# Performance work log

Measured on AMD Instinct MI355X. Metric: run time of the kernel, lower is better.

Reference implementation:

```python
import jax, jax.numpy as jnp
import numpy as np

N = 20000      # nodes
E = 160000     # edges
IN = 128       # in_channels
H = 16         # heads
C = 32         # hidden_channels (per-head dim)
HC = H * C     # 512
ED = 93        # edge_dim
B = 64         # graphs in batch


def setup_inputs() -> dict:
    key = jax.random.key(0)
    ks = jax.random.split(key, 32)
    w = lambda i, shape: jax.random.normal(ks[i], shape, dtype=jnp.float32) * 0.05
    inp = {
        "x": jax.random.normal(ks[0], (N, IN), dtype=jnp.float32),
        "edge_attr": jax.random.normal(ks[1], (E, ED), dtype=jnp.float32),
        "edge_index": jax.random.randint(ks[2], (2, E), 0, N),
        # sorted batch assignment; every graph id 0..B-1 is present
        "batch": (jnp.arange(N) * B) // N,
        # transformer1: in=IN
        "t1_Wq": w(3, (IN, HC)), "t1_bq": jnp.zeros((HC,), jnp.float32),
        "t1_Wk": w(4, (IN, HC)), "t1_bk": jnp.zeros((HC,), jnp.float32),
        "t1_Wv": w(5, (IN, HC)), "t1_bv": jnp.zeros((HC,), jnp.float32),
        "t1_We": w(6, (ED, HC)),
        "t1_Ws": w(7, (IN, HC)), "t1_bs": jnp.zeros((HC,), jnp.float32),
        # transformer2: in=HC
        "t2_Wq": w(8, (HC, HC)), "t2_bq": jnp.zeros((HC,), jnp.float32),
        "t2_Wk": w(9, (HC, HC)), "t2_bk": jnp.zeros((HC,), jnp.float32),
        "t2_Wv": w(10, (HC, HC)), "t2_bv": jnp.zeros((HC,), jnp.float32),
        "t2_We": w(11, (ED, HC)),
        "t2_Ws": w(12, (HC, HC)), "t2_bs": jnp.zeros((HC,), jnp.float32),
        # MLP head: fc1 (hidden*32 -> hidden*8), fc2 (hidden*8 -> hidden)
        "fc1_W": w(13, (2 * HC, 8 * C)), "fc1_b": jnp.zeros((8 * C,), jnp.float32),
        "fc2_W": w(14, (8 * C, C)), "fc2_b": jnp.zeros((C,), jnp.float32),
    }
    return inp


def _tconv(x, src, dst, edge_attr, Wq, bq, Wk, bk, Wv, bv, We, Ws, bs):
    # PyG TransformerConv, concat=True, beta=False, root_weight=True
    n = x.shape[0]
    q = (x @ Wq + bq).reshape(n, H, C)
    k = (x @ Wk + bk).reshape(n, H, C)
    v = (x @ Wv + bv).reshape(n, H, C)
    e = (edge_attr @ We).reshape(-1, H, C)          # lin_edge has no bias
    kj = k[src] + e                                  # [E,H,C]
    alpha = jnp.einsum('ehc,ehc->eh', q[dst], kj) / jnp.sqrt(jnp.float32(C))
    # segment softmax over incoming edges of each destination node
    amax = jax.ops.segment_max(alpha, dst, num_segments=n)
    ex = jnp.exp(alpha - amax[dst])
    denom = jax.ops.segment_sum(ex, dst, num_segments=n)
    a = ex / denom[dst]                              # [E,H]
    msg = (v[src] + e) * a[:, :, None]               # [E,H,C]
    agg = jax.ops.segment_sum(msg.reshape(-1, HC), dst, num_segments=n)
    return agg + x @ Ws + bs                         # root/skip connection


def _pool(x, batch):
    counts = jax.ops.segment_sum(jnp.ones((x.shape[0],), x.dtype), batch, num_segments=B)
    mean = jax.ops.segment_sum(x, batch, num_segments=B) / jnp.maximum(counts, 1.0)[:, None]
    mx = jax.ops.segment_max(x, batch, num_segments=B)
    return jnp.concatenate([mean, mx], axis=1)


def reference(x, edge_attr, edge_index, batch,
              t1_Wq, t1_bq, t1_Wk, t1_bk, t1_Wv, t1_bv, t1_We, t1_Ws, t1_bs,
              t2_Wq, t2_bq, t2_Wk, t2_bk, t2_Wv, t2_bv, t2_We, t2_Ws, t2_bs,
              fc1_W, fc1_b, fc2_W, fc2_b):
    src, dst = edge_index[0], edge_index[1]
    x1 = jax.nn.leaky_relu(_tconv(x, src, dst, edge_attr,
                                  t1_Wq, t1_bq, t1_Wk, t1_bk, t1_Wv, t1_bv,
                                  t1_We, t1_Ws, t1_bs), negative_slope=0.2)
    x3 = _pool(x1, batch)
    x2 = jax.nn.leaky_relu(_tconv(x1, src, dst, edge_attr,
                                  t2_Wq, t2_bq, t2_Wk, t2_bk, t2_Wv, t2_bv,
                                  t2_We, t2_Ws, t2_bs), negative_slope=0.2)
    x4 = _pool(x2, batch)
    h = x3 + x4                                      # [B, 2*HC]
    h = jax.nn.relu(h @ fc1_W + fc1_b)               # dropout = identity (eval)
    out = h @ fc2_W + fc2_b                          # [B, C]
    return out
```

## Files before the change

### kernel.cpp

```cpp
#include <hip/hip_runtime.h>
#include <cstdint>
#include <cstddef>

#define N_NODES 20000
#define N_EDGES 160000
#define IN_CH   128
#define NH      16
#define CD      32
#define HC      512
#define ED      93
#define EDP     96
#define NB      64
#define NCAT    2048
#define NSLICE  8

typedef __attribute__((ext_vector_type(8))) short short8;
typedef __attribute__((ext_vector_type(4))) float f32x4;
typedef unsigned short ushort_t;


__device__ inline ushort_t f2bf(float f) {
    unsigned int u = __float_as_uint(f);
    u = (u + 0x7FFF + ((u >> 16) & 1)) >> 16;
    return (ushort_t)u;
}
__device__ inline float bf2f(ushort_t u) {
    return __uint_as_float((unsigned)u << 16);
}
__device__ inline void unpack8(uint4 u, float* o) {
    o[0] = bf2f((ushort_t)(u.x & 0xffff)); o[1] = bf2f((ushort_t)(u.x >> 16));
    o[2] = bf2f((ushort_t)(u.y & 0xffff)); o[3] = bf2f((ushort_t)(u.y >> 16));
    o[4] = bf2f((ushort_t)(u.z & 0xffff)); o[5] = bf2f((ushort_t)(u.z >> 16));
    o[6] = bf2f((ushort_t)(u.w & 0xffff)); o[7] = bf2f((ushort_t)(u.w >> 16));
}
__device__ inline uint4 packf8(const float* f) {
    uint4 u;
    u.x = (unsigned)f2bf(f[0]) | ((unsigned)f2bf(f[1]) << 16);
    u.y = (unsigned)f2bf(f[2]) | ((unsigned)f2bf(f[3]) << 16);
    u.z = (unsigned)f2bf(f[4]) | ((unsigned)f2bf(f[5]) << 16);
    u.w = (unsigned)f2bf(f[6]) | ((unsigned)f2bf(f[7]) << 16);
    return u;
}

__device__ inline void gload_lds16(const void* g, void* l) {
    __builtin_amdgcn_global_load_lds(
        (const __attribute__((address_space(1))) void*)g,
        (__attribute__((address_space(3))) void*)l, 16, 0, 0);
}

__global__ void k_fill(float* __restrict__ p, float v, int n) {
    int i = blockIdx.x * blockDim.x + threadIdx.x;
    int stride = gridDim.x * blockDim.x;
    for (; i < n; i += stride) p[i] = v;
}
__global__ void k_zero_i(int* __restrict__ p, int n) {
    int i = blockIdx.x * blockDim.x + threadIdx.x;
    int stride = gridDim.x * blockDim.x;
    for (; i < n; i += stride) p[i] = 0;
}

__global__ void k_cvt_x(const float* __restrict__ in, ushort_t* __restrict__ out, int n8) {
    int i = blockIdx.x * blockDim.x + threadIdx.x;
    int stride = gridDim.x * blockDim.x;
    for (; i < n8; i += stride) {
        const float4* p = (const float4*)(in + (size_t)i * 8);
        float4 a = p[0], b = p[1];
        float f[8] = {a.x, a.y, a.z, a.w, b.x, b.y, b.z, b.w};
        *(uint4*)(out + (size_t)i * 8) = packf8(f);
    }
}

__global__ void k_cvt_ea(const float* __restrict__ in, ushort_t* __restrict__ out) {
    int i = blockIdx.x * blockDim.x + threadIdx.x;
    int stride = gridDim.x * blockDim.x;
    int total = N_EDGES * EDP;
    for (; i < total; i += stride) {
        int m = i / EDP, k = i - m * EDP;
        out[i] = (k < ED) ? f2bf(in[(size_t)m * ED + k]) : (ushort_t)0;
    }
}

__global__ __launch_bounds__(256) void k_cvt_wtT(
    const float* __restrict__ W0, const float* __restrict__ W1,
    const float* __restrict__ W2, const float* __restrict__ W3,
    ushort_t* __restrict__ Wt, int K, int N, int Kp) {
    __shared__ float tile[32][33];
    int z = blockIdx.z;
    const float* W = (z == 0) ? W0 : (z == 1) ? W1 : (z == 2) ? W2 : W3;
    ushort_t* out = Wt + (size_t)z * N * Kp;
    int n0 = blockIdx.x << 5;
    int k0 = blockIdx.y << 5;
    int r = threadIdx.x >> 5;
    int c = threadIdx.x & 31;
#pragma unroll
    for (int rr = 0; rr < 4; ++rr) {
        int k = k0 + r + rr * 8;
        tile[r + rr * 8][c] = (k < K) ? W[(size_t)k * N + n0 + c] : 0.f;
    }
    __syncthreads();
#pragma unroll
    for (int rr = 0; rr < 4; ++rr) {
        int n = n0 + r + rr * 8;
        out[(size_t)n * Kp + k0 + c] = f2bf(tile[c][r + rr * 8]);
    }
}

__global__ void k_bcat2(
    const float* __restrict__ b0q, const float* __restrict__ b0k,
    const float* __restrict__ b0v, const float* __restrict__ b0s,
    const float* __restrict__ b1q, const float* __restrict__ b1k,
    const float* __restrict__ b1v, const float* __restrict__ b1s,
    float* __restrict__ out) {
    int i = blockIdx.x * blockDim.x + threadIdx.x;
    if (i >= 2 * NCAT) return;
    int l = i >> 11, j = i & (NCAT - 1);
    int s = j >> 9, jj = j & 511;
    const float* b = (l == 0)
        ? ((s == 0) ? b0q : (s == 1) ? b0k : (s == 2) ? b0v : b0s)
        : ((s == 0) ? b1q : (s == 1) ? b1k : (s == 2) ? b1v : b1s);
    out[i] = b[jj];
}


__global__ void k_hist(const int* __restrict__ dst, int* __restrict__ deg) {
    int i = blockIdx.x * blockDim.x + threadIdx.x;
    if (i < N_EDGES) atomicAdd(&deg[dst[i]], 1);
}

__global__ __launch_bounds__(1024) void k_scan(const int* __restrict__ deg,
                                               int* __restrict__ rowptr,
                                               int* __restrict__ cursor) {
    __shared__ int part[1024];
    int t = threadIdx.x;
    int base = t * 20;
    int loc[20];
    int s = 0;
#pragma unroll
    for (int i = 0; i < 20; ++i) {
        int idx = base + i;
        int v = (idx < N_NODES) ? deg[idx] : 0;
        loc[i] = s; s += v;
    }
    part[t] = s;
    __syncthreads();
    for (int off = 1; off < 1024; off <<= 1) {
        int v = (t >= off) ? part[t - off] : 0;
        __syncthreads();
        part[t] += v;
        __syncthreads();
    }
    int pre = (t > 0) ? part[t - 1] : 0;
#pragma unroll
    for (int i = 0; i < 20; ++i) {
        int idx = base + i;
        if (idx < N_NODES) {
            int v = pre + loc[i];
            rowptr[idx] = v;
            cursor[idx] = v;
        }
    }
    if (t == 1023) rowptr[N_NODES] = part[1023];
}

__global__ void k_scatter(const int* __restrict__ src, const int* __restrict__ dst,
                          int* __restrict__ cursor, int* __restrict__ perm,
                          int* __restrict__ psrc) {
    int i = blockIdx.x * blockDim.x + threadIdx.x;
    if (i >= N_EDGES) return;
    int d = dst[i];
    int p = atomicAdd(&cursor[d], 1);
    perm[p] = i;
    psrc[p] = src[i];
}


__global__ __launch_bounds__(256) void k_mfma_gemm(
    const ushort_t* __restrict__ A, const ushort_t* __restrict__ Bt,
    const float* __restrict__ bias, ushort_t* __restrict__ Yb,
    int M, int K, int N) {
    __shared__ char smem[32768];
    char* As = smem;
    char* Bs = smem + 16384;

    int tid  = threadIdx.x;
    int lane = tid & 63, wave = tid >> 6;
    int l15 = lane & 15, lg = lane >> 4;
    int nt = N >> 7;
    int nwg = gridDim.x;
    int bid = blockIdx.x;
    int wg;
    if ((nwg & 7) == 0) { int cpx = nwg >> 3; wg = (bid & 7) * cpx + (bid >> 3); }
    else wg = bid;
    int bm = (wg / nt) * 128, bn = (wg % nt) * 128;
    int wm = (wave >> 1) * 64, wn = (wave & 1) * 64;

    f32x4 acc[4][4] = {};

    int sr = lane >> 3;
    int su = lane & 7;
    int gu = su ^ sr;

    for (int k0 = 0; k0 < K; k0 += 64) {
#pragma unroll
        for (int i = 0; i < 4; ++i) {
            int rloc = wave * 32 + i * 8;
            int row = rloc + sr;
            if (bm + row < M)
                gload_lds16(A + (size_t)(bm + row) * K + k0 + gu * 8, As + rloc * 128);
            gload_lds16(Bt + (size_t)(bn + row) * K + k0 + gu * 8, Bs + rloc * 128);
        }
        __syncthreads();

#pragma unroll
        for (int ks = 0; ks < 2; ++ks) {
            short8 af[4], bfr[4];
#pragma unroll
            for (int mr = 0; mr < 4; ++mr) {
                int r = wm + mr * 16 + l15;
                af[mr] = *(const short8*)(As + r * 128 + (((ks * 4 + lg) ^ (r & 7)) << 4));
            }
#pragma unroll
            for (int nc = 0; nc < 4; ++nc) {
                int r = wn + nc * 16 + l15;
                bfr[nc] = *(const short8*)(Bs + r * 128 + (((ks * 4 + lg) ^ (r & 7)) << 4));
            }
#pragma unroll
            for (int mr = 0; mr < 4; ++mr)
#pragma unroll
                for (int nc = 0; nc < 4; ++nc)
                    acc[mr][nc] = __builtin_amdgcn_mfma_f32_16x16x32_bf16(
                        af[mr], bfr[nc], acc[mr][nc], 0, 0, 0);
        }
        __syncthreads();
    }

    char* Cs = smem;
#pragma unroll
    for (int mr = 0; mr < 4; ++mr) {
#pragma unroll
        for (int nc = 0; nc < 4; ++nc) {
            int coll = wn + nc * 16 + l15;
            float b = bias ? bias[bn + coll] : 0.f;
            int u0 = coll >> 3;
#pragma unroll
            for (int j = 0; j < 4; ++j) {
                int row = wm + mr * 16 + lg * 4 + j;
                int u = u0 ^ (row & 7);
                *(ushort_t*)(Cs + row * 256 + (u << 4) + ((coll & 7) << 1)) =
                    f2bf(acc[mr][nc][j] + b);
            }
        }
    }
    __syncthreads();
    {
        int rsub = tid >> 4;
        int un   = tid & 15;
#pragma unroll
        for (int i = 0; i < 8; ++i) {
            int row = i * 16 + rsub;
            int gr = bm + row;
            if (gr < M) {
                int u = un ^ (row & 7);
                *(uint4*)(Yb + (size_t)gr * N + bn + un * 8) =
                    *(const uint4*)(Cs + row * 256 + (u << 4));
            }
        }
    }
}


__global__ __launch_bounds__(256) void k_egemm(
    const ushort_t* __restrict__ Ab, const ushort_t* __restrict__ Bt,
    ushort_t* __restrict__ Yb, const int* __restrict__ perm,
    int pbase, int ec) {
    __shared__ char smem[49152];
    char* As = smem;
    char* Bs = smem + 24576;

    int tid  = threadIdx.x;
    int lane = tid & 63, wave = tid >> 6;
    int l15 = lane & 15, lg = lane >> 4;
    int nwg = gridDim.x;
    int bid = blockIdx.x;
    int wg;
    if ((nwg & 7) == 0) { int cpx = nwg >> 3; wg = (bid & 7) * cpx + (bid >> 3); }
    else wg = bid;
    int bm = (wg >> 2) * 128;
    int n0 = (wg & 3) * 128;
    int wm = (wave >> 1) * 64, wn = (wave & 1) * 64;

    int srow = tid >> 1;
    int h    = tid & 1;
    int ssw  = ((srow >> 1) & 3) << 4;
    {
        int gm = bm + srow;
        uint4 va[6];
#pragma unroll
        for (int i = 0; i < 6; ++i) { va[i].x = va[i].y = va[i].z = va[i].w = 0; }
        if (gm < ec) {
            int ar = perm[pbase + gm];
            const uint4* ga = (const uint4*)(Ab + (size_t)ar * EDP + h * 48);
#pragma unroll
            for (int i = 0; i < 6; ++i) va[i] = ga[i];
        }
        char* dsta = As + srow * 192;
#pragma unroll
        for (int i = 0; i < 6; ++i) {
            int c = h * 96 + i * 16;
            *(uint4*)(dsta + ((c & ~63) | ((c & 63) ^ ssw))) = va[i];
        }
        uint4 vb[6];
        {
            const uint4* gb = (const uint4*)(Bt + (size_t)(n0 + srow) * EDP + h * 48);
#pragma unroll
            for (int i = 0; i < 6; ++i) vb[i] = gb[i];
        }
        char* dstb = Bs + srow * 192;
#pragma unroll
        for (int i = 0; i < 6; ++i) {
            int c = h * 96 + i * 16;
            *(uint4*)(dstb + ((c & ~63) | ((c & 63) ^ ssw))) = vb[i];
        }
    }
    __syncthreads();

    int fsw = ((l15 >> 1) & 3) << 4;

    f32x4 acc[4][4] = {};
#pragma unroll
    for (int ks = 0; ks < 3; ++ks) {
        short8 af[4], bfr[4];
#pragma unroll
        for (int mr = 0; mr < 4; ++mr) {
            int r = wm + mr * 16 + l15;
            int c = ks * 64 + ((lg * 16) ^ fsw);
            af[mr] = *(const short8*)(As + r * 192 + c);
        }
#pragma unroll
        for (int nc = 0; nc < 4; ++nc) {
            int r = wn + nc * 16 + l15;
            int c = ks * 64 + ((lg * 16) ^ fsw);
            bfr[nc] = *(const short8*)(Bs + r * 192 + c);
        }
#pragma unroll
        for (int mr = 0; mr < 4; ++mr)
#pragma unroll
            for (int nc = 0; nc < 4; ++nc)
                acc[mr][nc] = __builtin_amdgcn_mfma_f32_16x16x32_bf16(
                    af[mr], bfr[nc], acc[mr][nc], 0, 0, 0);
    }
    __syncthreads();

    char* Cs = smem;
#pragma unroll
    for (int mr = 0; mr < 4; ++mr) {
#pragma unroll
        for (int nc = 0; nc < 4; ++nc) {
            int col = wn + nc * 16 + l15;
#pragma unroll
            for (int j = 0; j < 4; ++j) {
                int row = wm + mr * 16 + lg * 4 + j;
                *(ushort_t*)(Cs + row * 288 + col * 2) = f2bf(acc[mr][nc][j]);
            }
        }
    }
    __syncthreads();

    {
        int rsub = tid >> 4;
        int un   = tid & 15;
#pragma unroll
        for (int i = 0; i < 8; ++i) {
            int row = i * 16 + rsub;
            if (bm + row < ec) {
                *(uint4*)(Yb + (size_t)(bm + row) * HC + n0 + un * 8) =
                    *(const uint4*)(Cs + row * 288 + un * 16);
            }
        }
    }
}


__global__ __launch_bounds__(128) void k_edge_f(
    const ushort_t* __restrict__ qkvs, const ushort_t* __restrict__ eb,
    const int* __restrict__ psrc, const int* __restrict__ rowptr,
    ushort_t* __restrict__ xoutb) {
    int n = blockIdx.x;
    int beg = rowptr[n], end = rowptr[n + 1];

    int t = threadIdx.x;
    int w = t >> 6;
    int lane = t & 63;
    int c0 = lane * 8;
    int h = lane >> 2;

    float q[8];
    unpack8(*(const uint4*)(qkvs + (size_t)n * NCAT + c0), q);

    float mm = -1e30f, dd = 0.f, a[8];
#pragma unroll
    for (int j = 0; j < 8; ++j) a[j] = 0.f;

    int i = beg + w;
    uint4 ku4, vu4, eu4;
    if (i < end) {
        int sn = psrc[i];
        ku4 = *(const uint4*)(qkvs + (size_t)sn * NCAT + 512 + c0);
        vu4 = *(const uint4*)(qkvs + (size_t)sn * NCAT + 1024 + c0);
        eu4 = *(const uint4*)(eb + (size_t)i * HC + c0);
    }
    while (i < end) {
        uint4 kc = ku4, vc = vu4, ec = eu4;
        int inext = i + 2;
        if (inext < end) {
            int sn2 = psrc[inext];
            ku4 = *(const uint4*)(qkvs + (size_t)sn2 * NCAT + 512 + c0);
            vu4 = *(const uint4*)(qkvs + (size_t)sn2 * NCAT + 1024 + c0);
            eu4 = *(const uint4*)(eb + (size_t)inext * HC + c0);
        }
        float kk[8], vv[8], ee[8];
        unpack8(kc, kk); unpack8(vc, vv); unpack8(ec, ee);
        float part = 0.f;
#pragma unroll
        for (int j = 0; j < 8; ++j) part += q[j] * (kk[j] + ee[j]);
        part += __shfl_xor(part, 1);
        part += __shfl_xor(part, 2);
        float s = part * 0.17677669529663687f;
        float mn = fmaxf(mm, s);
        float sc = __expf(mm - mn);
        float p  = __expf(s - mn);
        dd = dd * sc + p;
        mm = mn;
#pragma unroll
        for (int j = 0; j < 8; ++j) a[j] = a[j] * sc + p * (vv[j] + ee[j]);
        i = inext;
    }

    __shared__ float sm_acc[512];
    __shared__ float sm_m[16];
    __shared__ float sm_d[16];
    if (w == 1) {
#pragma unroll
        for (int j = 0; j < 8; ++j) sm_acc[c0 + j] = a[j];
        if ((lane & 3) == 0) { sm_m[h] = mm; sm_d[h] = dd; }
    }
    __syncthreads();
    if (w == 0) {
        float m1 = sm_m[h], d1 = sm_d[h];
        float M = fmaxf(mm, m1);
        float sc0 = __expf(mm - M);
        float sc1 = __expf(m1 - M);
        dd = dd * sc0 + d1 * sc1;
        float inv = (dd > 0.f) ? 1.f / dd : 0.f;
        float sk[8];
        unpack8(*(const uint4*)(qkvs + (size_t)n * NCAT + 1536 + c0), sk);
        float o[8];
#pragma unroll
        for (int j = 0; j < 8; ++j) {
            float msg = (a[j] * sc0 + sm_acc[c0 + j] * sc1) * inv;
            float v = msg + sk[j];
            o[j] = v >= 0.f ? v : 0.2f * v;
        }
        *(uint4*)(xoutb + (size_t)n * HC + c0) = packf8(o);
    }
}

__global__ __launch_bounds__(128) void k_edge(
    const ushort_t* __restrict__ qkvs, const ushort_t* __restrict__ eb,
    const int* __restrict__ psrc, const int* __restrict__ rowptr,
    float* __restrict__ macc, float* __restrict__ mbuf, float* __restrict__ dbuf,
    int e0, int e1) {
    int n = blockIdx.x;
    int beg = rowptr[n], end = rowptr[n + 1];
    int lo = beg > e0 ? beg : e0;
    int hi = end < e1 ? end : e1;
    if (lo >= hi) return;

    int t = threadIdx.x;
    int w = t >> 6;
    int lane = t & 63;
    int c0 = lane * 8;
    int h = lane >> 2;
    bool fresh = (beg >= e0);

    float q[8];
    unpack8(*(const uint4*)(qkvs + (size_t)n * NCAT + c0), q);

    float mm, dd, a[8];
    if (w == 0 && !fresh) {
        mm = mbuf[n * NH + h];
        dd = dbuf[n * NH + h];
        float4 a0 = *(const float4*)(macc + (size_t)n * HC + c0);
        float4 a1 = *(const float4*)(macc + (size_t)n * HC + c0 + 4);
        a[0] = a0.x; a[1] = a0.y; a[2] = a0.z; a[3] = a0.w;
        a[4] = a1.x; a[5] = a1.y; a[6] = a1.z; a[7] = a1.w;
    } else {
        mm = -1e30f; dd = 0.f;
#pragma unroll
        for (int j = 0; j < 8; ++j) a[j] = 0.f;
    }

    int i = lo + w;
    uint4 ku4, vu4, eu4;
    if (i < hi) {
        int sn = psrc[i];
        ku4 = *(const uint4*)(qkvs + (size_t)sn * NCAT + 512 + c0);
        vu4 = *(const uint4*)(qkvs + (size_t)sn * NCAT + 1024 + c0);
        eu4 = *(const uint4*)(eb + (size_t)(i - e0) * HC + c0);
    }
    while (i < hi) {
        uint4 kc = ku4, vc = vu4, ec = eu4;
        int inext = i + 2;
        if (inext < hi) {
            int sn2 = psrc[inext];
            ku4 = *(const uint4*)(qkvs + (size_t)sn2 * NCAT + 512 + c0);
            vu4 = *(const uint4*)(qkvs + (size_t)sn2 * NCAT + 1024 + c0);
            eu4 = *(const uint4*)(eb + (size_t)(inext - e0) * HC + c0);
        }
        float kk[8], vv[8], ee[8];
        unpack8(kc, kk); unpack8(vc, vv); unpack8(ec, ee);
        float part = 0.f;
#pragma unroll
        for (int j = 0; j < 8; ++j) part += q[j] * (kk[j] + ee[j]);
        part += __shfl_xor(part, 1);
        part += __shfl_xor(part, 2);
        float s = part * 0.17677669529663687f;
        float mn = fmaxf(mm, s);
        float sc = __expf(mm - mn);
        float p  = __expf(s - mn);
        dd = dd * sc + p;
        mm = mn;
#pragma unroll
        for (int j = 0; j < 8; ++j) a[j] = a[j] * sc + p * (vv[j] + ee[j]);
        i = inext;
    }

    __shared__ float sm_acc[512];
    __shared__ float sm_m[16];
    __shared__ float sm_d[16];
    if (w == 1) {
#pragma unroll
        for (int j = 0; j < 8; ++j) sm_acc[c0 + j] = a[j];
        if ((lane & 3) == 0) { sm_m[h] = mm; sm_d[h] = dd; }
    }
    __syncthreads();
    if (w == 0) {
        float m1 = sm_m[h], d1 = sm_d[h];
        float M = fmaxf(mm, m1);
        float sc0 = __expf(mm - M);
        float sc1 = __expf(m1 - M);
        dd = dd * sc0 + d1 * sc1;
        float4 o0, o1;
        o0.x = a[0] * sc0 + sm_acc[c0 + 0] * sc1;
        o0.y = a[1] * sc0 + sm_acc[c0 + 1] * sc1;
        o0.z = a[2] * sc0 + sm_acc[c0 + 2] * sc1;
        o0.w = a[3] * sc0 + sm_acc[c0 + 3] * sc1;
        o1.x = a[4] * sc0 + sm_acc[c0 + 4] * sc1;
        o1.y = a[5] * sc0 + sm_acc[c0 + 5] * sc1;
        o1.z = a[6] * sc0 + sm_acc[c0 + 6] * sc1;
        o1.w = a[7] * sc0 + sm_acc[c0 + 7] * sc1;
        *(float4*)(macc + (size_t)n * HC + c0) = o0;
        *(float4*)(macc + (size_t)n * HC + c0 + 4) = o1;
        if ((lane & 3) == 0) { mbuf[n * NH + h] = M; dbuf[n * NH + h] = dd; }
    }
}

__global__ void k_epi2(const float* __restrict__ macc, const float* __restrict__ dbuf,
                       const ushort_t* __restrict__ qkvs, ushort_t* __restrict__ xoutb,
                       int n) {
    int i = blockIdx.x * blockDim.x + threadIdx.x;
    int stride = gridDim.x * blockDim.x;
    for (; i < n; i += stride) {
        int node = i >> 9, c = i & (HC - 1);
        int h = c >> 5;
        float dd = dbuf[node * NH + h];
        float msg = (dd > 0.f) ? macc[i] / dd : 0.f;
        float sk = bf2f(qkvs[(size_t)node * NCAT + 1536 + c]);
        float v = msg + sk;
        v = v >= 0.f ? v : 0.2f * v;
        xoutb[i] = f2bf(v);
    }
}


__global__ __launch_bounds__(256) void k_pool2(
    const ushort_t* __restrict__ xb, const int* __restrict__ batch,
    float* __restrict__ psum_p, float* __restrict__ pmax_p, int* __restrict__ cnt) {
    int b = blockIdx.x;
    int s = blockIdx.y;
    int lo = 0, hi = N_NODES;
    while (lo < hi) { int mid = (lo + hi) >> 1; if (batch[mid] < b) lo = mid + 1; else hi = mid; }
    int beg = lo;
    hi = N_NODES;
    while (lo < hi) { int mid = (lo + hi) >> 1; if (batch[mid] < b + 1) lo = mid + 1; else hi = mid; }
    int end = lo;
    if (s == 0 && threadIdx.x == 0) cnt[b] = end - beg;
    int cn = end - beg;
    int per = (cn + NSLICE - 1) / NSLICE;
    int nb = beg + s * per;
    int ne = nb + per; if (ne > end) ne = end;
    int c0 = threadIdx.x * 2;
    float s0 = 0.f, s1 = 0.f, m0 = -1e30f, m1 = -1e30f;
    for (int n = nb; n < ne; ++n) {
        unsigned int v = *(const unsigned int*)(xb + (size_t)n * HC + c0);
        float v0 = bf2f((ushort_t)(v & 0xffff));
        float v1 = bf2f((ushort_t)(v >> 16));
        s0 += v0; s1 += v1;
        m0 = fmaxf(m0, v0); m1 = fmaxf(m1, v1);
    }
    size_t o = ((size_t)s * NB + b) * HC + c0;
    psum_p[o] = s0; psum_p[o + 1] = s1;
    pmax_p[o] = m0; pmax_p[o + 1] = m1;
}

__global__ void k_poolfin(const float* __restrict__ psum_p, const float* __restrict__ pmax_p,
                          const int* __restrict__ cnt, float* __restrict__ hsum, int mode) {
    int i = blockIdx.x * blockDim.x + threadIdx.x;
    if (i >= NB * 1024) return;
    int b = i >> 10, c = i & 1023;
    float val;
    if (c < HC) {
        float s = 0.f;
#pragma unroll
        for (int sl = 0; sl < NSLICE; ++sl)
            s += psum_p[((size_t)sl * NB + b) * HC + c];
        int ct = cnt[b];
        val = s / (float)(ct > 0 ? ct : 1);
    } else {
        int cc = c - HC;
        float m = -1e30f;
#pragma unroll
        for (int sl = 0; sl < NSLICE; ++sl)
            m = fmaxf(m, pmax_p[((size_t)sl * NB + b) * HC + cc]);
        val = m;
    }
    if (mode == 0) hsum[i] = val;
    else hsum[i] += val;
}


__global__ __launch_bounds__(256) void k_head(
    const float* __restrict__ hsum, const float* __restrict__ fc1W,
    const float* __restrict__ fc1b, const float* __restrict__ fc2W,
    const float* __restrict__ fc2b, float* __restrict__ out) {
    int b = blockIdx.x;
    int j = threadIdx.x;
    __shared__ float hs[256];
    float acc = fc1b[j];
    const float* hin = hsum + (size_t)b * 1024;
    for (int k = 0; k < 1024; ++k) {
        acc += hin[k] * fc1W[(size_t)k * 256 + j];
    }
    hs[j] = fmaxf(acc, 0.f);
    __syncthreads();
    if (j < 32) {
        float o = fc2b[j];
        for (int k = 0; k < 256; ++k) o += hs[k] * fc2W[(size_t)k * 32 + j];
        out[b * 32 + j] = o;
    }
}


extern "C" void kernel_launch(void* const* d_in, const int* in_sizes, int n_in,
                              void* d_out, int out_size, void* d_ws, size_t ws_size,
                              hipStream_t stream) {
    const float* x      = (const float*)d_in[0];
    const float* ea     = (const float*)d_in[1];
    const int*   ei     = (const int*)d_in[2];
    const int*   batch  = (const int*)d_in[3];
    const int* src = ei;
    const int* dst = ei + N_EDGES;

    const float* t1_Wq = (const float*)d_in[4];
    const float* t1_bq = (const float*)d_in[5];
    const float* t1_Wk = (const float*)d_in[6];
    const float* t1_bk = (const float*)d_in[7];
    const float* t1_Wv = (const float*)d_in[8];
    const float* t1_bv = (const float*)d_in[9];
    const float* t1_We = (const float*)d_in[10];
    const float* t1_Ws = (const float*)d_in[11];
    const float* t1_bs = (const float*)d_in[12];
    const float* t2_Wq = (const float*)d_in[13];
    const float* t2_bq = (const float*)d_in[14];
    const float* t2_Wk = (const float*)d_in[15];
    const float* t2_bk = (const float*)d_in[16];
    const float* t2_Wv = (const float*)d_in[17];
    const float* t2_bv = (const float*)d_in[18];
    const float* t2_We = (const float*)d_in[19];
    const float* t2_Ws = (const float*)d_in[20];
    const float* t2_bs = (const float*)d_in[21];
    const float* fc1_W = (const float*)d_in[22];
    const float* fc1_b = (const float*)d_in[23];
    const float* fc2_W = (const float*)d_in[24];
    const float* fc2_b = (const float*)d_in[25];

    char* ws = (char*)d_ws;
    size_t off = 0;
    auto alloc = [&](size_t bytes) -> void* {
        void* p = ws + off;
        off = (off + bytes + 255) & ~(size_t)255;
        return p;
    };

    ushort_t* qkvs = (ushort_t*)alloc((size_t)N_NODES * NCAT * 2);
    float* psum_p = (float*)alloc((size_t)NSLICE * NB * HC * 4);
    float* pmax_p = (float*)alloc((size_t)NSLICE * NB * HC * 4);
    float* hsum = (float*)alloc((size_t)NB * 1024 * 4);
    int*   cnt  = (int*)alloc((size_t)NB * 4);
    int* deg    = (int*)alloc((size_t)N_NODES * 4);
    int* rowptr = (int*)alloc((size_t)(N_NODES + 1) * 4);
    int* cursor = (int*)alloc((size_t)N_NODES * 4);
    int* perm   = (int*)alloc((size_t)N_EDGES * 4);
    int* psrc   = (int*)alloc((size_t)N_EDGES * 4);
    ushort_t* x_b  = (ushort_t*)alloc((size_t)N_NODES * IN_CH * 2);
    ushort_t* x1_b = (ushort_t*)alloc((size_t)N_NODES * HC * 2);
    ushort_t* ea_b = (ushort_t*)alloc((size_t)N_EDGES * EDP * 2);
    ushort_t* wcat1 = (ushort_t*)alloc((size_t)NCAT * IN_CH * 2);
    ushort_t* wcat2 = (ushort_t*)alloc((size_t)NCAT * HC * 2);
    ushort_t* w_e   = (ushort_t*)alloc((size_t)2 * HC * EDP * 2);
    float* bcat = (float*)alloc((size_t)2 * NCAT * 4);

    size_t need_eb = (size_t)N_EDGES * HC * 2;
    size_t remain = (ws_size > off) ? (ws_size - off) : 0;
    bool full = (remain >= need_eb);
    ushort_t* eb;
    float* macc = nullptr; float* mbuf = nullptr; float* dbuf = nullptr;
    int EC;
    if (full) {
        eb = (ushort_t*)alloc(need_eb);
        EC = N_EDGES;
    } else {
        macc = (float*)alloc((size_t)N_NODES * HC * 4);
        mbuf = (float*)alloc((size_t)N_NODES * NH * 4);
        dbuf = (float*)alloc((size_t)N_NODES * NH * 4);
        remain = (ws_size > off) ? (ws_size - off) : 0;
        eb = (ushort_t*)(ws + off);
        size_t per_edge = (size_t)HC * 2;
        EC = (int)(remain / per_edge);
        EC &= ~255;
        if (EC <= 0) EC = 256;
        if (EC > N_EDGES) EC = N_EDGES;
    }
    (void)in_sizes; (void)n_in; (void)out_size;

    const int NHC = N_NODES * HC;

    hipLaunchKernelGGL(k_zero_i, dim3(79), dim3(256), 0, stream, deg, N_NODES);
    hipLaunchKernelGGL(k_hist, dim3((N_EDGES + 255) / 256), dim3(256), 0, stream, dst, deg);
    hipLaunchKernelGGL(k_scan, dim3(1), dim3(1024), 0, stream, deg, rowptr, cursor);
    hipLaunchKernelGGL(k_scatter, dim3((N_EDGES + 255) / 256), dim3(256), 0, stream,
                       src, dst, cursor, perm, psrc);

    hipLaunchKernelGGL(k_cvt_x, dim3(512), dim3(256), 0, stream, x, x_b,
                       N_NODES * IN_CH / 8);
    hipLaunchKernelGGL(k_cvt_ea, dim3(4096), dim3(256), 0, stream, ea, ea_b);
    hipLaunchKernelGGL(k_cvt_wtT, dim3(HC / 32, IN_CH / 32, 4), dim3(256), 0, stream,
                       t1_Wq, t1_Wk, t1_Wv, t1_Ws, wcat1, IN_CH, HC, IN_CH);
    hipLaunchKernelGGL(k_cvt_wtT, dim3(HC / 32, HC / 32, 4), dim3(256), 0, stream,
                       t2_Wq, t2_Wk, t2_Wv, t2_Ws, wcat2, HC, HC, HC);
    hipLaunchKernelGGL(k_cvt_wtT, dim3(HC / 32, EDP / 32, 2), dim3(256), 0, stream,
                       t1_We, t2_We, t1_We, t1_We, w_e, ED, HC, EDP);
    hipLaunchKernelGGL(k_bcat2, dim3(16), dim3(256), 0, stream,
                       t1_bq, t1_bk, t1_bv, t1_bs, t2_bq, t2_bk, t2_bv, t2_bs, bcat);

    auto run_layer = [&](const ushort_t* xin_b, int Kin, const ushort_t* wcat,
                         const float* bc, const ushort_t* we,
                         ushort_t* xoutb, int poolmode) {
        int mt = (N_NODES + 127) / 128;
        int nt = NCAT / 128;
        int nq = mt * nt;
        hipLaunchKernelGGL(k_mfma_gemm, dim3(nq), dim3(256), 0, stream,
                           xin_b, wcat, bc, qkvs, N_NODES, Kin, NCAT);

        if (full) {
            int gm = (N_EDGES + 127) / 128;
            hipLaunchKernelGGL(k_egemm, dim3(gm * 4), dim3(256), 0, stream,
                               ea_b, we, eb, perm, 0, N_EDGES);
            hipLaunchKernelGGL(k_edge_f, dim3(N_NODES), dim3(128), 0, stream,
                               qkvs, eb, psrc, rowptr, xoutb);
        } else {
            hipLaunchKernelGGL(k_fill, dim3(512), dim3(256), 0, stream, dbuf, 0.f, N_NODES * NH);
            for (int e0 = 0; e0 < N_EDGES; e0 += EC) {
                int ec = (N_EDGES - e0 < EC) ? (N_EDGES - e0) : EC;
                int gm = (ec + 127) / 128;
                hipLaunchKernelGGL(k_egemm, dim3(gm * 4), dim3(256), 0, stream,
                                   ea_b, we, eb, perm, e0, ec);
                hipLaunchKernelGGL(k_edge, dim3(N_NODES), dim3(128), 0, stream,
                                   qkvs, eb, psrc, rowptr, macc, mbuf, dbuf, e0, e0 + ec);
            }
            hipLaunchKernelGGL(k_epi2, dim3(2048), dim3(256), 0, stream,
                               macc, dbuf, qkvs, xoutb, NHC);
        }

        hipLaunchKernelGGL(k_pool2, dim3(NB, NSLICE), dim3(256), 0, stream,
                           xoutb, batch, psum_p, pmax_p, cnt);
        hipLaunchKernelGGL(k_poolfin, dim3((NB * 1024 + 255) / 256), dim3(256), 0, stream,
                           psum_p, pmax_p, cnt, hsum, poolmode);
    };

    run_layer(x_b, IN_CH, wcat1, bcat, w_e, x1_b, 0);
    run_layer(x1_b, HC, wcat2, bcat + NCAT, w_e + (size_t)HC * EDP, x1_b, 1);

    hipLaunchKernelGGL(k_head, dim3(NB), dim3(256), 0, stream,
                       hsum, fc1_W, fc1_b, fc2_W, fc2_b, (float*)d_out);
}
```

Before: 633.0 us.

## Merge node QKVS GEMM and edge-attribute GEMM into one launch

Adds a combined kernel whose first blocks compute the node Q/K/V/skip projection GEMM and whose remaining blocks compute the permuted edge-attribute projection GEMM, replacing two separate launches in the full path. The intent is to fill the GPU with both independent workloads at once, so the small node GEMM's tail overlaps with edge GEMM blocks, and to remove one launch gap. Shared memory per block grows to 48KB for all blocks, which may reduce occupancy for the node GEMM portion.

```diff
diff --git a/kernel.cpp b/kernel.cpp
--- a/kernel.cpp
+++ b/kernel.cpp
@@ -171,6 +171,203 @@
     int p = atomicAdd(&cursor[d], 1);
     perm[p] = i;
     psrc[p] = src[i];
+}
+
+
+__global__ __launch_bounds__(256) void k_mega(
+    const ushort_t* __restrict__ A, const ushort_t* __restrict__ Bt,
+    const float* __restrict__ bias, ushort_t* __restrict__ Yb,
+    int M, int K, int N, int nq,
+    const ushort_t* __restrict__ Ab, const ushort_t* __restrict__ Bte,
+    ushort_t* __restrict__ Ybe, const int* __restrict__ perm, int neg) {
+    __shared__ char smem[49152];
+    int tid  = threadIdx.x;
+    int lane = tid & 63, wave = tid >> 6;
+    int l15 = lane & 15, lg = lane >> 4;
+    int wm = (wave >> 1) * 64, wn = (wave & 1) * 64;
+
+    if (blockIdx.x < nq) {
+        char* As = smem;
+        char* Bs = smem + 16384;
+        int nt = N >> 7;
+        int bid = blockIdx.x;
+        int wg;
+        if ((nq & 7) == 0) { int cpx = nq >> 3; wg = (bid & 7) * cpx + (bid >> 3); }
+        else wg = bid;
+        int bm = (wg / nt) * 128, bn = (wg % nt) * 128;
+
+        f32x4 acc[4][4] = {};
+
+        int sr = lane >> 3;
+        int su = lane & 7;
+        int gu = su ^ sr;
+
+        for (int k0 = 0; k0 < K; k0 += 64) {
+#pragma unroll
+            for (int i = 0; i < 4; ++i) {
+                int rloc = wave * 32 + i * 8;
+                int row = rloc + sr;
+                if (bm + row < M)
+                    gload_lds16(A + (size_t)(bm + row) * K + k0 + gu * 8, As + rloc * 128);
+                gload_lds16(Bt + (size_t)(bn + row) * K + k0 + gu * 8, Bs + rloc * 128);
+            }
+            __syncthreads();
+
+#pragma unroll
+            for (int ks = 0; ks < 2; ++ks) {
+                short8 af[4], bfr[4];
+#pragma unroll
+                for (int mr = 0; mr < 4; ++mr) {
+                    int r = wm + mr * 16 + l15;
+                    af[mr] = *(const short8*)(As + r * 128 + (((ks * 4 + lg) ^ (r & 7)) << 4));
+                }
+#pragma unroll
+                for (int nc = 0; nc < 4; ++nc) {
+                    int r = wn + nc * 16 + l15;
+                    bfr[nc] = *(const short8*)(Bs + r * 128 + (((ks * 4 + lg) ^ (r & 7)) << 4));
+                }
+#pragma unroll
+                for (int mr = 0; mr < 4; ++mr)
+#pragma unroll
+                    for (int nc = 0; nc < 4; ++nc)
+                        acc[mr][nc] = __builtin_amdgcn_mfma_f32_16x16x32_bf16(
+                            af[mr], bfr[nc], acc[mr][nc], 0, 0, 0);
+            }
+            __syncthreads();
+        }
+
+        char* Cs = smem;
+#pragma unroll
+        for (int mr = 0; mr < 4; ++mr) {
+#pragma unroll
+            for (int nc = 0; nc < 4; ++nc) {
+                int coll = wn + nc * 16 + l15;
+                float b = bias ? bias[bn + coll] : 0.f;
+                int u0 = coll >> 3;
+#pragma unroll
+                for (int j = 0; j < 4; ++j) {
+                    int row = wm + mr * 16 + lg * 4 + j;
+                    int u = u0 ^ (row & 7);
+                    *(ushort_t*)(Cs + row * 256 + (u << 4) + ((coll & 7) << 1)) =
+                        f2bf(acc[mr][nc][j] + b);
+                }
+            }
+        }
+        __syncthreads();
+        {
+            int rsub = tid >> 4;
+            int un   = tid & 15;
+#pragma unroll
+            for (int i = 0; i < 8; ++i) {
+                int row = i * 16 + rsub;
+                int gr = bm + row;
+                if (gr < M) {
+                    int u = un ^ (row & 7);
+                    *(uint4*)(Yb + (size_t)gr * N + bn + un * 8) =
+                        *(const uint4*)(Cs + row * 256 + (u << 4));
+                }
+            }
+        }
+    } else {
+        char* As = smem;
+        char* Bs = smem + 24576;
+        int bid = blockIdx.x - nq;
+        int wg;
+        if ((neg & 7) == 0) { int cpx = neg >> 3; wg = (bid & 7) * cpx + (bid >> 3); }
+        else wg = bid;
+        int bm = (wg >> 2) * 128;
+        int n0 = (wg & 3) * 128;
+
+        int srow = tid >> 1;
+        int h    = tid & 1;
+        int ssw  = ((srow >> 1) & 3) << 4;
+        {
+            int gm = bm + srow;
+            uint4 va[6];
+#pragma unroll
+            for (int i = 0; i < 6; ++i) { va[i].x = va[i].y = va[i].z = va[i].w = 0; }
+            if (gm < N_EDGES) {
+                int ar = perm[gm];
+                const uint4* ga = (const uint4*)(Ab + (size_t)ar * EDP + h * 48);
+#pragma unroll
+                for (int i = 0; i < 6; ++i) va[i] = ga[i];
+            }
+            char* dsta = As + srow * 192;
+#pragma unroll
+            for (int i = 0; i < 6; ++i) {
+                int c = h * 96 + i * 16;
+                *(uint4*)(dsta + ((c & ~63) | ((c & 63) ^ ssw))) = va[i];
+            }
+            uint4 vb[6];
+            {
+                const uint4* gb = (const uint4*)(Bte + (size_t)(n0 + srow) * EDP + h * 48);
+#pragma unroll
+                for (int i = 0; i < 6; ++i) vb[i] = gb[i];
+            }
+            char* dstb = Bs + srow * 192;
+#pragma unroll
+            for (int i = 0; i < 6; ++i) {
+                int c = h * 96 + i * 16;
+                *(uint4*)(dstb + ((c & ~63) | ((c & 63) ^ ssw))) = vb[i];
+            }
+        }
+        __syncthreads();
+
+        int fsw = ((l15 >> 1) & 3) << 4;
+
+        f32x4 acc[4][4] = {};
+#pragma unroll
+        for (int ks = 0; ks < 3; ++ks) {
+            short8 af[4], bfr[4];
+#pragma unroll
+            for (int mr = 0; mr < 4; ++mr) {
+                int r = wm + mr * 16 + l15;
+                int c = ks * 64 + ((lg * 16) ^ fsw);
+                af[mr] = *(const short8*)(As + r * 192 + c);
+            }
+#pragma unroll
+            for (int nc = 0; nc < 4; ++nc) {
+                int r = wn + nc * 16 + l15;
+                int c = ks * 64 + ((lg * 16) ^ fsw);
+                bfr[nc] = *(const short8*)(Bs + r * 192 + c);
+            }
+#pragma unroll
+            for (int mr = 0; mr < 4; ++mr)
+#pragma unroll
+                for (int nc = 0; nc < 4; ++nc)
+                    acc[mr][nc] = __builtin_amdgcn_mfma_f32_16x16x32_bf16(
+                        af[mr], bfr[nc], acc[mr][nc], 0, 0, 0);
+        }
+        __syncthreads();
+
+        char* Cs = smem;
+#pragma unroll
+        for (int mr = 0; mr < 4; ++mr) {
+#pragma unroll
+            for (int nc = 0; nc < 4; ++nc) {
+                int col = wn + nc * 16 + l15;
+#pragma unroll
+                for (int j = 0; j < 4; ++j) {
+                    int row = wm + mr * 16 + lg * 4 + j;
+                    *(ushort_t*)(Cs + row * 288 + col * 2) = f2bf(acc[mr][nc][j]);
+                }
+            }
+        }
+        __syncthreads();
+
+        {
+            int rsub = tid >> 4;
+            int un   = tid & 15;
+#pragma unroll
+            for (int i = 0; i < 8; ++i) {
+                int row = i * 16 + rsub;
+                if (bm + row < N_EDGES) {
+                    *(uint4*)(Ybe + (size_t)(bm + row) * HC + n0 + un * 8) =
+                        *(const uint4*)(Cs + row * 288 + un * 16);
+                }
+            }
+        }
+    }
 }
 
 
@@ -769,16 +966,17 @@
         int mt = (N_NODES + 127) / 128;
         int nt = NCAT / 128;
         int nq = mt * nt;
-        hipLaunchKernelGGL(k_mfma_gemm, dim3(nq), dim3(256), 0, stream,
-                           xin_b, wcat, bc, qkvs, N_NODES, Kin, NCAT);
 
         if (full) {
-            int gm = (N_EDGES + 127) / 128;
-            hipLaunchKernelGGL(k_egemm, dim3(gm * 4), dim3(256), 0, stream,
-                               ea_b, we, eb, perm, 0, N_EDGES);
+            int neg = ((N_EDGES + 127) / 128) * 4;
+            hipLaunchKernelGGL(k_mega, dim3(nq + neg), dim3(256), 0, stream,
+                               xin_b, wcat, bc, qkvs, N_NODES, Kin, NCAT, nq,
+                               ea_b, we, eb, perm, neg);
             hipLaunchKernelGGL(k_edge_f, dim3(N_NODES), dim3(128), 0, stream,
                                qkvs, eb, psrc, rowptr, xoutb);
         } else {
+            hipLaunchKernelGGL(k_mfma_gemm, dim3(nq), dim3(256), 0, stream,
+                               xin_b, wcat, bc, qkvs, N_NODES, Kin, NCAT);
             hipLaunchKernelGGL(k_fill, dim3(512), dim3(256), 0, stream, dbuf, 0.f, N_NODES * NH);
             for (int e0 = 0; e0 < N_EDGES; e0 += EC) {
                 int ec = (N_EDGES - e0 < EC) ? (N_EDGES - e0) : EC;
```

Result: no change. 634.1 us (+0.2%).

## Chunk edges by destination-node ownership so the single-pass edge kernel always runs

Applied to the files above, without the earlier changes.

Replaces the low-workspace fallback, which partially accumulated softmax state in fp32 node buffers across edge chunks and finished with a separate epilogue. Edges are now split into chunks aligned to destination-node ownership, with a slack of extra edge rows so every node's incoming edges fall in one chunk. This lets the fused single-pass edge kernel finish each node directly and drops the fill and epilogue kernels and the fp32 accumulator traffic. It recomputes slack edge rows per chunk, and it assumes no node has more incoming edges than the slack allows. When the workspace already holds all edge rows, behaviour is essentially unchanged.

```diff
diff --git a/kernel.cpp b/kernel.cpp
--- a/kernel.cpp
+++ b/kernel.cpp
@@ -13,6 +13,7 @@
 #define NB      64
 #define NCAT    2048
 #define NSLICE  8
+#define DEGSLK  8192
 
 typedef __attribute__((ext_vector_type(8))) short short8;
 typedef __attribute__((ext_vector_type(4))) float f32x4;
@@ -48,11 +49,6 @@
         (__attribute__((address_space(3))) void*)l, 16, 0, 0);
 }
 
-__global__ void k_fill(float* __restrict__ p, float v, int n) {
-    int i = blockIdx.x * blockDim.x + threadIdx.x;
-    int stride = gridDim.x * blockDim.x;
-    for (; i < n; i += stride) p[i] = v;
-}
 __global__ void k_zero_i(int* __restrict__ p, int n) {
     int i = blockIdx.x * blockDim.x + threadIdx.x;
     int stride = gridDim.x * blockDim.x;
@@ -381,12 +377,13 @@
 }
 
 
-__global__ __launch_bounds__(128) void k_edge_f(
+__global__ __launch_bounds__(128) void k_edge_fc(
     const ushort_t* __restrict__ qkvs, const ushort_t* __restrict__ eb,
     const int* __restrict__ psrc, const int* __restrict__ rowptr,
-    ushort_t* __restrict__ xoutb) {
+    ushort_t* __restrict__ xoutb, int e0, int elim) {
     int n = blockIdx.x;
     int beg = rowptr[n], end = rowptr[n + 1];
+    if (beg < e0 || beg >= elim) return;
 
     int t = threadIdx.x;
     int w = t >> 6;
@@ -407,7 +404,7 @@
         int sn = psrc[i];
         ku4 = *(const uint4*)(qkvs + (size_t)sn * NCAT + 512 + c0);
         vu4 = *(const uint4*)(qkvs + (size_t)sn * NCAT + 1024 + c0);
-        eu4 = *(const uint4*)(eb + (size_t)i * HC + c0);
+        eu4 = *(const uint4*)(eb + (size_t)(i - e0) * HC + c0);
     }
     while (i < end) {
         uint4 kc = ku4, vc = vu4, ec = eu4;
@@ -416,7 +413,7 @@
             int sn2 = psrc[inext];
             ku4 = *(const uint4*)(qkvs + (size_t)sn2 * NCAT + 512 + c0);
             vu4 = *(const uint4*)(qkvs + (size_t)sn2 * NCAT + 1024 + c0);
-            eu4 = *(const uint4*)(eb + (size_t)inext * HC + c0);
+            eu4 = *(const uint4*)(eb + (size_t)(inext - e0) * HC + c0);
         }
         float kk[8], vv[8], ee[8];
         unpack8(kc, kk); unpack8(vc, vv); unpack8(ec, ee);
@@ -462,123 +459,6 @@
             o[j] = v >= 0.f ? v : 0.2f * v;
         }
         *(uint4*)(xoutb + (size_t)n * HC + c0) = packf8(o);
-    }
-}
-
-__global__ __launch_bounds__(128) void k_edge(
-    const ushort_t* __restrict__ qkvs, const ushort_t* __restrict__ eb,
-    const int* __restrict__ psrc, const int* __restrict__ rowptr,
-    float* __restrict__ macc, float* __restrict__ mbuf, float* __restrict__ dbuf,
-    int e0, int e1) {
-    int n = blockIdx.x;
-    int beg = rowptr[n], end = rowptr[n + 1];
-    int lo = beg > e0 ? beg : e0;
-    int hi = end < e1 ? end : e1;
-    if (lo >= hi) return;
-
-    int t = threadIdx.x;
-    int w = t >> 6;
-    int lane = t & 63;
-    int c0 = lane * 8;
-    int h = lane >> 2;
-    bool fresh = (beg >= e0);
-
-    float q[8];
-    unpack8(*(const uint4*)(qkvs + (size_t)n * NCAT + c0), q);
-
-    float mm, dd, a[8];
-    if (w == 0 && !fresh) {
-        mm = mbuf[n * NH + h];
-        dd = dbuf[n * NH + h];
-        float4 a0 = *(const float4*)(macc + (size_t)n * HC + c0);
-        float4 a1 = *(const float4*)(macc + (size_t)n * HC + c0 + 4);
-        a[0] = a0.x; a[1] = a0.y; a[2] = a0.z; a[3] = a0.w;
-        a[4] = a1.x; a[5] = a1.y; a[6] = a1.z; a[7] = a1.w;
-    } else {
-        mm = -1e30f; dd = 0.f;
-#pragma unroll
-        for (int j = 0; j < 8; ++j) a[j] = 0.f;
-    }
-
-    int i = lo + w;
-    uint4 ku4, vu4, eu4;
-    if (i < hi) {
-        int sn = psrc[i];
-        ku4 = *(const uint4*)(qkvs + (size_t)sn * NCAT + 512 + c0);
-        vu4 = *(const uint4*)(qkvs + (size_t)sn * NCAT + 1024 + c0);
-        eu4 = *(const uint4*)(eb + (size_t)(i - e0) * HC + c0);
-    }
-    while (i < hi) {
-        uint4 kc = ku4, vc = vu4, ec = eu4;
-        int inext = i + 2;
-        if (inext < hi) {
-            int sn2 = psrc[inext];
-            ku4 = *(const uint4*)(qkvs + (size_t)sn2 * NCAT + 512 + c0);
-            vu4 = *(const uint4*)(qkvs + (size_t)sn2 * NCAT + 1024 + c0);
-            eu4 = *(const uint4*)(eb + (size_t)(inext - e0) * HC + c0);
-        }
-        float kk[8], vv[8], ee[8];
-        unpack8(kc, kk); unpack8(vc, vv); unpack8(ec, ee);
-        float part = 0.f;
-#pragma unroll
-        for (int j = 0; j < 8; ++j) part += q[j] * (kk[j] + ee[j]);
-        part += __shfl_xor(part, 1);
-        part += __shfl_xor(part, 2);
-        float s = part * 0.17677669529663687f;
-        float mn = fmaxf(mm, s);
-        float sc = __expf(mm - mn);
-        float p  = __expf(s - mn);
-        dd = dd * sc + p;
-        mm = mn;
-#pragma unroll
-        for (int j = 0; j < 8; ++j) a[j] = a[j] * sc + p * (vv[j] + ee[j]);
-        i = inext;
-    }
-
-    __shared__ float sm_acc[512];
-    __shared__ float sm_m[16];
-    __shared__ float sm_d[16];
-    if (w == 1) {
-#pragma unroll
-        for (int j = 0; j < 8; ++j) sm_acc[c0 + j] = a[j];
-        if ((lane & 3) == 0) { sm_m[h] = mm; sm_d[h] = dd; }
-    }
-    __syncthreads();
-    if (w == 0) {
-        float m1 = sm_m[h], d1 = sm_d[h];
-        float M = fmaxf(mm, m1);
-        float sc0 = __expf(mm - M);
-        float sc1 = __expf(m1 - M);
-        dd = dd * sc0 + d1 * sc1;
-        float4 o0, o1;
-        o0.x = a[0] * sc0 + sm_acc[c0 + 0] * sc1;
-        o0.y = a[1] * sc0 + sm_acc[c0 + 1] * sc1;
-        o0.z = a[2] * sc0 + sm_acc[c0 + 2] * sc1;
-        o0.w = a[3] * sc0 + sm_acc[c0 + 3] * sc1;
-        o1.x = a[4] * sc0 + sm_acc[c0 + 4] * sc1;
-        o1.y = a[5] * sc0 + sm_acc[c0 + 5] * sc1;
-        o1.z = a[6] * sc0 + sm_acc[c0 + 6] * sc1;
-        o1.w = a[7] * sc0 + sm_acc[c0 + 7] * sc1;
-        *(float4*)(macc + (size_t)n * HC + c0) = o0;
-        *(float4*)(macc + (size_t)n * HC + c0 + 4) = o1;
-        if ((lane & 3) == 0) { mbuf[n * NH + h] = M; dbuf[n * NH + h] = dd; }
-    }
-}
-
-__global__ void k_epi2(const float* __restrict__ macc, const float* __restrict__ dbuf,
-                       const ushort_t* __restrict__ qkvs, ushort_t* __restrict__ xoutb,
-                       int n) {
-    int i = blockIdx.x * blockDim.x + threadIdx.x;
-    int stride = gridDim.x * blockDim.x;
-    for (; i < n; i += stride) {
-        int node = i >> 9, c = i & (HC - 1);
-        int h = c >> 5;
-        float dd = dbuf[node * NH + h];
-        float msg = (dd > 0.f) ? macc[i] / dd : 0.f;
-        float sk = bf2f(qkvs[(size_t)node * NCAT + 1536 + c]);
-        float v = msg + sk;
-        v = v >= 0.f ? v : 0.2f * v;
-        xoutb[i] = f2bf(v);
     }
 }
 
@@ -720,30 +600,16 @@
     ushort_t* w_e   = (ushort_t*)alloc((size_t)2 * HC * EDP * 2);
     float* bcat = (float*)alloc((size_t)2 * NCAT * 4);
 
-    size_t need_eb = (size_t)N_EDGES * HC * 2;
     size_t remain = (ws_size > off) ? (ws_size - off) : 0;
-    bool full = (remain >= need_eb);
-    ushort_t* eb;
-    float* macc = nullptr; float* mbuf = nullptr; float* dbuf = nullptr;
-    int EC;
-    if (full) {
-        eb = (ushort_t*)alloc(need_eb);
-        EC = N_EDGES;
-    } else {
-        macc = (float*)alloc((size_t)N_NODES * HC * 4);
-        mbuf = (float*)alloc((size_t)N_NODES * NH * 4);
-        dbuf = (float*)alloc((size_t)N_NODES * NH * 4);
-        remain = (ws_size > off) ? (ws_size - off) : 0;
-        eb = (ushort_t*)(ws + off);
-        size_t per_edge = (size_t)HC * 2;
-        EC = (int)(remain / per_edge);
-        EC &= ~255;
-        if (EC <= 0) EC = 256;
-        if (EC > N_EDGES) EC = N_EDGES;
-    }
+    ushort_t* eb = (ushort_t*)(ws + off);
+    size_t per_edge = (size_t)HC * 2;
+    long cap_rows = (long)(remain / per_edge);
+    long S_max = cap_rows - DEGSLK;
+    if (S_max < 1024) S_max = 1024;
+    int nch = (int)((N_EDGES + S_max - 1) / S_max);
+    if (nch < 1) nch = 1;
+    int S = (N_EDGES + nch - 1) / nch;
     (void)in_sizes; (void)n_in; (void)out_size;
-
-    const int NHC = N_NODES * HC;
 
     hipLaunchKernelGGL(k_zero_i, dim3(79), dim3(256), 0, stream, deg, N_NODES);
     hipLaunchKernelGGL(k_hist, dim3((N_EDGES + 255) / 256), dim3(256), 0, stream, dst, deg);
@@ -768,28 +634,21 @@
                          ushort_t* xoutb, int poolmode) {
         int mt = (N_NODES + 127) / 128;
         int nt = NCAT / 128;
-        int nq = mt * nt;
-        hipLaunchKernelGGL(k_mfma_gemm, dim3(nq), dim3(256), 0, stream,
+        hipLaunchKernelGGL(k_mfma_gemm, dim3(mt * nt), dim3(256), 0, stream,
                            xin_b, wcat, bc, qkvs, N_NODES, Kin, NCAT);
 
-        if (full) {
-            int gm = (N_EDGES + 127) / 128;
+        for (int ci = 0; ci < nch; ++ci) {
+            int e0 = ci * S;
+            if (e0 >= N_EDGES) break;
+            long ecl = (long)S + DEGSLK;
+            if (ecl > N_EDGES - e0) ecl = N_EDGES - e0;
+            int ecnt = (int)ecl;
+            int gm = (ecnt + 127) / 128;
             hipLaunchKernelGGL(k_egemm, dim3(gm * 4), dim3(256), 0, stream,
-                               ea_b, we, eb, perm, 0, N_EDGES);
-            hipLaunchKernelGGL(k_edge_f, dim3(N_NODES), dim3(128), 0, stream,
-                               qkvs, eb, psrc, rowptr, xoutb);
-        } else {
-            hipLaunchKernelGGL(k_fill, dim3(512), dim3(256), 0, stream, dbuf, 0.f, N_NODES * NH);
-            for (int e0 = 0; e0 < N_EDGES; e0 += EC) {
-                int ec = (N_EDGES - e0 < EC) ? (N_EDGES - e0) : EC;
-                int gm = (ec + 127) / 128;
-                hipLaunchKernelGGL(k_egemm, dim3(gm * 4), dim3(256), 0, stream,
-                                   ea_b, we, eb, perm, e0, ec);
-                hipLaunchKernelGGL(k_edge, dim3(N_NODES), dim3(128), 0, stream,
-                                   qkvs, eb, psrc, rowptr, macc, mbuf, dbuf, e0, e0 + ec);
-            }
-            hipLaunchKernelGGL(k_epi2, dim3(2048), dim3(256), 0, stream,
-                               macc, dbuf, qkvs, xoutb, NHC);
+                               ea_b, we, eb, perm, e0, ecnt);
+            int elim = (ci == nch - 1) ? (N_EDGES + 1) : (e0 + S);
+            hipLaunchKernelGGL(k_edge_fc, dim3(N_NODES), dim3(128), 0, stream,
+                               qkvs, eb, psrc, rowptr, xoutb, e0, elim);
         }
 
         hipLaunchKernelGGL(k_pool2, dim3(NB, NSLICE), dim3(256), 0, stream,
```

New measurement: 567.5 us. -10.3%, faster.
